# Kernel tuning notes

Hardware: AMD Instinct MI355X
Metric: run time of the kernel (lower is better)

Reference implementation:

```python
import jax, jax.numpy as jnp
import numpy as np

N = 512            # input_size == number of graph nodes (X = I_N)
B = 64             # batch_size
H1, H2, H3 = 128, 64, 32   # hidden3 + 16 must equal 32 + class_nums
OUT = 8            # output_size; OUT*OUT + OUT == 72 (controller out channels)
CLS = 16           # class_nums (one-hot task encoding is 16-dim)


def setup_inputs():
    key = jax.random.key(0)
    ks = jax.random.split(key, 20)

    def u(k, shape, fan_out):
        s = 1.0 / np.sqrt(fan_out)
        return jax.random.uniform(k, shape, jnp.float32, -s, s)

    inp = {
        "adj": jax.random.uniform(ks[0], (B, 2, N, N), jnp.float32),
        "task_id": jax.random.randint(ks[1], (B,), 0, CLS),
    }
    dims = [(N, H1), (H1, H2), (H2, H3), (H3, OUT)]
    i = 2
    for pref in ("p", "n"):
        for l, (fi, fo) in enumerate(dims, 1):
            inp[f"w{l}{pref}"] = u(ks[i], (fi, fo), fo); i += 1
            inp[f"b{l}{pref}"] = u(ks[i], (fo,), fo); i += 1
    # controller: Conv1d(H3+CLS, 72, kernel=1, bias=False) -> stored as [72, H3+CLS]
    inp["wc"] = jax.random.normal(ks[i], (OUT * OUT + OUT, H3 + CLS), jnp.float32) * np.sqrt(2.0 / (OUT * OUT + OUT))
    return inp


def _normalize(adj):
    # D^-1/2 (A + I) D^-1/2, fully vectorized over [B, 2] (original loops in Python)
    a = adj + jnp.eye(adj.shape[-1], dtype=adj.dtype)
    d = a.sum(-1) ** -0.5                       # [B,2,N]
    return d[..., :, None] * a * d[..., None, :]


def _leaky(x):
    return jnp.where(x >= 0, x, 0.2 * x)


def _gcn_branch(feat, ws, bs):
    # feat: [B,N,N] normalized adjacency; X = I_N so first support = W1
    x = jnp.eye(N, dtype=feat.dtype)
    for i, (w, b) in enumerate(zip(ws, bs)):
        x = jnp.matmul(feat, jnp.matmul(x, w)) + b   # [B,N,fo]
        if i < len(ws) - 1:
            x = _leaky(x)
        if i == len(ws) - 2:
            conv3 = x
    return conv3, x                                  # ([B,N,H3], [B,N,OUT])


def _dcl(conv3, task_enc, conv4, wc):
    # conv3: [B,N,H3]; conv4: [B,N,OUT]; task_enc: [B,CLS]
    x_feat = conv3.mean(axis=1)                       # AdaptiveAvgPool1d over nodes -> [B,H3]
    x_cond = jnp.concatenate([x_feat, task_enc], 1)   # [B,H3+CLS]
    params = x_cond @ wc.T                            # [B,72]
    w = params[:, :OUT * OUT].reshape(B, OUT, OUT)    # per-sample dynamic head weights
    b = params[:, OUT * OUT:]                         # [B,OUT]
    # head_inputs = conv4.view(1,-1,N) with groups=B grouped conv1d (kernel 1)
    head = conv4.reshape(B, OUT, N)
    logits = jnp.einsum('boi,bin->bon', w, head) + b[..., None]   # [B,OUT,N]
    return logits.reshape(B, N, OUT)                  # faithful to torch reshape(N_,H_,-1)


def _forward(adj, task_id, w1p, b1p, w2p, b2p, w3p, b3p, w4p, b4p,
             w1n, b1n, w2n, b2n, w3n, b3n, w4n, b4n, wc):
    adj_n = _normalize(adj)
    feat_p, feat_n = adj_n[:, 0], adj_n[:, 1]
    p3, p4 = _gcn_branch(feat_p, [w1p, w2p, w3p, w4p], [b1p, b2p, b3p, b4p])
    n3, n4 = _gcn_branch(feat_n, [w1n, w2n, w3n, w4n], [b1n, b2n, b3n, b4n])
    te = jax.nn.one_hot(task_id, CLS, dtype=adj.dtype)   # encoding_task
    lp = _dcl(p3, te, p4, wc)
    ln = _dcl(n3, te, n4, wc)
    cc = jnp.concatenate([lp, ln], -1).reshape(-1, 2, N, OUT)  # [B,2,N,OUT]
    # F.dropout treated as identity (eval-mode determinism for reference)
    xm = jnp.matmul(cc, jnp.swapaxes(cc, -1, -2))              # [B,2,N,N]
    return jax.nn.log_sigmoid(xm) * -1.0


def reference(adj, task_id, w1p, b1p, w2p, b2p, w3p, b3p, w4p, b4p,
              w1n, b1n, w2n, b2n, w3n, b3n, w4n, b4n, wc):
    return _forward(adj, task_id, w1p, b1p, w2p, b2p, w3p, b3p, w4p, b4p,
                    w1n, b1n, w2n, b2n, w3n, b3n, w4n, b4n, wc)
```

## Files before the change

### kernel.cpp

```cpp
#include <hip/hip_runtime.h>
#include <math.h>

#define NN 512
#define NBC 128

typedef __attribute__((ext_vector_type(8))) __bf16 v8bf;
typedef __attribute__((ext_vector_type(4))) float v4f;

__device__ __forceinline__ void bsplit(float v, unsigned short& h, unsigned short& l) {
    unsigned u  = __builtin_bit_cast(unsigned, v);
    unsigned hb = (u + 0x7fffu + ((u >> 16) & 1u)) & 0xffff0000u;
    float hf    = __builtin_bit_cast(float, hb);
    h = (unsigned short)(hb >> 16);
    float lof   = v - hf;
    unsigned ul = __builtin_bit_cast(unsigned, lof);
    l = (unsigned short)((ul + 0x7fffu + ((ul >> 16) & 1u)) >> 16);
}

__global__ __launch_bounds__(256) void k_rowsum(const float* __restrict__ adj,
                                                float* __restrict__ dinv) {
    int wave = blockIdx.x * 4 + (threadIdx.x >> 6);
    int lane = threadIdx.x & 63;
    const float4* row = (const float4*)(adj + (size_t)wave * NN);
    float4 v0 = row[lane], v1 = row[lane + 64];
    float s = v0.x + v0.y + v0.z + v0.w + v1.x + v1.y + v1.z + v1.w;
    #pragma unroll
    for (int off = 32; off; off >>= 1) s += __shfl_down(s, off, 64);
    if (lane == 0) dinv[wave] = rsqrtf(1.0f + s);
}

__global__ __launch_bounds__(256) void k_convert(const float* __restrict__ adj,
    const float* __restrict__ dinv, unsigned short* __restrict__ anh,
    unsigned short* __restrict__ anl)
{
    unsigned gid = blockIdx.x * 256 + threadIdx.x;
    unsigned e = gid * 4;
    unsigned bc = e >> 18, rem = e & 0x3ffffu;
    unsigned i = rem >> 9, j = rem & 511u;
    float4 a = *(const float4*)(adj + (size_t)e);
    float di = dinv[bc * NN + i];
    const float4 dj = *(const float4*)(dinv + bc * NN + j);
    float v0 = di * dj.x * (a.x + ((j + 0) == i ? 1.f : 0.f));
    float v1 = di * dj.y * (a.y + ((j + 1) == i ? 1.f : 0.f));
    float v2 = di * dj.z * (a.z + ((j + 2) == i ? 1.f : 0.f));
    float v3 = di * dj.w * (a.w + ((j + 3) == i ? 1.f : 0.f));
    ushort4 hh, ll;
    bsplit(v0, hh.x, ll.x); bsplit(v1, hh.y, ll.y);
    bsplit(v2, hh.z, ll.z); bsplit(v3, hh.w, ll.w);
    *(ushort4*)(anh + e) = hh;
    *(ushort4*)(anl + e) = ll;
}

struct WJob  { const float* w; unsigned short* dh; unsigned short* dl; int HI; int HO; int HOP; };
struct WJobs { WJob j[8]; };
__global__ __launch_bounds__(256) void k_wprep(WJobs jobs) {
    WJob jb = jobs.j[blockIdx.y];
    int idx = blockIdx.x * 256 + threadIdx.x;
    if (idx >= jb.HOP * jb.HI) return;
    int h = idx / jb.HI, p = idx % jb.HI;
    float v = (h < jb.HO) ? jb.w[p * jb.HO + h] : 0.f;
    unsigned short hh, ll; bsplit(v, hh, ll);
    jb.dh[idx] = hh; jb.dl[idx] = ll;
}

template<int BN, int OUTW, bool SHAREDZ, bool ACT, bool WBF>
__global__ __launch_bounds__(256, 2) void k_mfma(
    const unsigned short* __restrict__ anh_, const unsigned short* __restrict__ anl_,
    const unsigned short* __restrict__ zh_,  const unsigned short* __restrict__ zl_,
    const float* __restrict__ bp, const float* __restrict__ bn,
    float* __restrict__ xf, unsigned short* __restrict__ xh, unsigned short* __restrict__ xl)
{
    constexpr int C = BN / 16;
    const int bc = blockIdx.y, rb = blockIdx.x;
    const int t = threadIdx.x, w = t >> 6, lane = t & 63;
    const int m0 = lane & 15, quad = lane >> 4;
    const int rowbase = rb * 128 + w * 32;
    const int s = SHAREDZ ? (bc & 1) : bc;
    const unsigned short* pa_h = anh_ + ((size_t)bc * NN + rowbase + m0) * NN + quad * 8;
    const unsigned short* pa_l = anl_ + ((size_t)bc * NN + rowbase + m0) * NN + quad * 8;
    const unsigned short* pz_h = zh_ + ((size_t)s * BN + m0) * NN + quad * 8;
    const unsigned short* pz_l = zl_ + ((size_t)s * BN + m0) * NN + quad * 8;
    v4f acc[2][C];
    #pragma unroll
    for (int r = 0; r < 2; ++r)
        #pragma unroll
        for (int c = 0; c < C; ++c) acc[r][c] = (v4f){0.f, 0.f, 0.f, 0.f};

    for (int kb = 0; kb < 16; ++kb) {
        const int ko = kb * 32;
        v8bf zfh[C], zfl[C];
        #pragma unroll
        for (int c = 0; c < C; ++c) {
            zfh[c] = *(const v8bf*)(pz_h + (size_t)(c * 16) * NN + ko);
            zfl[c] = *(const v8bf*)(pz_l + (size_t)(c * 16) * NN + ko);
        }
        #pragma unroll
        for (int r = 0; r < 2; ++r) {
            v8bf ah = *(const v8bf*)(pa_h + (size_t)(r * 16) * NN + ko);
            v8bf al = *(const v8bf*)(pa_l + (size_t)(r * 16) * NN + ko);
            #pragma unroll
            for (int c = 0; c < C; ++c) {
                acc[r][c] = __builtin_amdgcn_mfma_f32_16x16x32_bf16(ah, zfh[c], acc[r][c], 0, 0, 0);
                acc[r][c] = __builtin_amdgcn_mfma_f32_16x16x32_bf16(ah, zfl[c], acc[r][c], 0, 0, 0);
                acc[r][c] = __builtin_amdgcn_mfma_f32_16x16x32_bf16(al, zfh[c], acc[r][c], 0, 0, 0);
            }
        }
    }
    const float* bias = (bc & 1) ? bn : bp;
    #pragma unroll
    for (int r = 0; r < 2; ++r)
        #pragma unroll
        for (int c = 0; c < C; ++c) {
            int col = c * 16 + m0;
            if (OUTW < BN && col >= OUTW) continue;
            float bv = bias[col];
            #pragma unroll
            for (int reg = 0; reg < 4; ++reg) {
                int row = rowbase + r * 16 + quad * 4 + reg;
                float v = acc[r][c][reg] + bv;
                if (ACT) v = v >= 0.f ? v : 0.2f * v;
                size_t oi = ((size_t)bc * NN + row) * OUTW + col;
                if (xf) xf[oi] = v;
                if (WBF) {
                    unsigned short hh, ll; bsplit(v, hh, ll);
                    xh[oi] = hh; xl[oi] = ll;
                }
            }
        }
}

template<int HI, int HOP>
__global__ __launch_bounds__(256) void k_zgemm(
    const unsigned short* __restrict__ wth, const unsigned short* __restrict__ wtl,
    const unsigned short* __restrict__ xh_, const unsigned short* __restrict__ xl_,
    unsigned short* __restrict__ zh_, unsigned short* __restrict__ zl_)
{
    constexpr int MT = HOP / 16, JW = 4 / MT, NT = 8 / JW;
    const int bc = blockIdx.y, jb = blockIdx.x;
    const int t = threadIdx.x, w = t >> 6, lane = t & 63;
    const int m0 = lane & 15, quad = lane >> 4;
    const int mt = w % MT, jseg = w / MT;
    const int n0 = jb * 128 + jseg * (128 / JW);
    const int s = bc & 1;
    const unsigned short* pw_h = wth + ((size_t)s * HOP + mt * 16 + m0) * HI + quad * 8;
    const unsigned short* pw_l = wtl + ((size_t)s * HOP + mt * 16 + m0) * HI + quad * 8;
    const unsigned short* px_h = xh_ + ((size_t)bc * NN + n0 + m0) * HI + quad * 8;
    const unsigned short* px_l = xl_ + ((size_t)bc * NN + n0 + m0) * HI + quad * 8;
    v4f acc[NT];
    #pragma unroll
    for (int c = 0; c < NT; ++c) acc[c] = (v4f){0.f, 0.f, 0.f, 0.f};
    #pragma unroll
    for (int ks = 0; ks < HI / 32; ++ks) {
        const int ko = ks * 32;
        v8bf awh = *(const v8bf*)(pw_h + ko);
        v8bf awl = *(const v8bf*)(pw_l + ko);
        #pragma unroll
        for (int c = 0; c < NT; ++c) {
            v8bf bxh = *(const v8bf*)(px_h + (size_t)(c * 16) * HI + ko);
            v8bf bxl = *(const v8bf*)(px_l + (size_t)(c * 16) * HI + ko);
            acc[c] = __builtin_amdgcn_mfma_f32_16x16x32_bf16(awh, bxh, acc[c], 0, 0, 0);
            acc[c] = __builtin_amdgcn_mfma_f32_16x16x32_bf16(awh, bxl, acc[c], 0, 0, 0);
            acc[c] = __builtin_amdgcn_mfma_f32_16x16x32_bf16(awl, bxh, acc[c], 0, 0, 0);
        }
    }
    #pragma unroll
    for (int c = 0; c < NT; ++c) {
        int j = n0 + c * 16 + m0;
        #pragma unroll
        for (int reg = 0; reg < 4; ++reg) {
            int h = mt * 16 + quad * 4 + reg;
            unsigned short hh, ll; bsplit(acc[c][reg], hh, ll);
            size_t oi = ((size_t)bc * HOP + h) * NN + j;
            zh_[oi] = hh; zl_[oi] = ll;
        }
    }
}

template<int H, int HP, bool SHARED, bool ACT>
__global__ __launch_bounds__(256) void k_biggemm(
    const float* __restrict__ adj, const float* __restrict__ zcg,
    const float* __restrict__ wp, const float* __restrict__ wn,
    const float* __restrict__ bp, const float* __restrict__ bn,
    const float* __restrict__ dinv, float* __restrict__ xout)
{
    constexpr int CPT = HP / 16;
    constexpr int KT = 64;
    __shared__ float a_s[64 * 68];
    __shared__ float z_s[KT * H];
    const int bc = blockIdx.y;
    const int rt = blockIdx.x;
    const int t  = threadIdx.x;
    const int tx = t & 15, ty = t >> 4;
    const float* A    = adj + (size_t)bc * NN * NN + (size_t)rt * 64 * NN;
    const float* dloc = dinv + bc * NN;
    const float* ZG   = SHARED ? ((bc & 1) ? wn : wp) : (zcg + (size_t)bc * NN * H);
    const float* bias = (bc & 1) ? bn : bp;
    float acc[4][CPT];
    #pragma unroll
    for (int r = 0; r < 4; ++r)
        #pragma unroll
        for (int u = 0; u < CPT; ++u) acc[r][u] = 0.f;
    for (int kb = 0; kb < NN; kb += KT) {
        __syncthreads();
        #pragma unroll
        for (int l = 0; l < 4; ++l) {
            int idx = t + l * 256;
            int r = idx >> 4, q = idx & 15;
            float4 v = *(const float4*)(A + (size_t)r * NN + kb + q * 4);
            *(float4*)(a_s + r * 68 + q * 4) = v;
        }
        constexpr int NZ4 = KT * H / 4;
        for (int idx = t; idx < NZ4; idx += 256) {
            int k = idx / (H / 4), hq = idx % (H / 4);
            float4 v = *(const float4*)(ZG + (size_t)(kb + k) * H + hq * 4);
            if (SHARED) {
                float dk = dloc[kb + k];
                v.x *= dk; v.y *= dk; v.z *= dk; v.w *= dk;
            }
            *(float4*)(z_s + k * H + hq * 4) = v;
        }
        __syncthreads();
        #pragma unroll 8
        for (int k = 0; k < KT; ++k) {
            float ar[4];
            #pragma unroll
            for (int r = 0; r < 4; ++r) ar[r] = a_s[(ty * 4 + r) * 68 + k];
            float zv[CPT];
            #pragma unroll
            for (int u = 0; u < CPT; ++u) {
                int h = tx * CPT + u;
                if (H < HP && h >= H) h = 0;
                zv[u] = z_s[k * H + h];
            }
            #pragma unroll
            for (int r = 0; r < 4; ++r)
                #pragma unroll
                for (int u = 0; u < CPT; ++u)
                    acc[r][u] += ar[r] * zv[u];
        }
    }
    #pragma unroll
    for (int r = 0; r < 4; ++r) {
        int i = rt * 64 + ty * 4 + r;
        float di = dloc[i];
        #pragma unroll
        for (int u = 0; u < CPT; ++u) {
            int h = tx * CPT + u;
            if (H < HP && h >= H) continue;
            float self = SHARED ? di * ZG[(size_t)i * H + h] : ZG[(size_t)i * H + h];
            float v = di * (acc[r][u] + self) + bias[h];
            if (ACT) v = v >= 0.f ? v : 0.2f * v;
            xout[((size_t)bc * NN + i) * H + h] = v;
        }
    }
}
// ... 86 lines not shown
        #pragma unroll
        for (int j = 0; j < 32; ++j) s += wr[j] * xf[j];
        pr[t] = s;
    }
    __syncthreads();
    const float* X4 = x4 + (size_t)bc * 4096;
    float* Lb = L + (size_t)bc * 4096;
    #pragma unroll
    for (int rep = 0; rep < 2; ++rep) {
        int n = rep * 256 + t;
        float hi[8];
        #pragma unroll
        for (int i = 0; i < 8; ++i) hi[i] = X4[i * 512 + n];
        #pragma unroll
        for (int o = 0; o < 8; ++o) {
            float s = pr[64 + o];
            #pragma unroll
            for (int i = 0; i < 8; ++i) s += pr[o * 8 + i] * hi[i];
            Lb[o * 512 + n] = s;
        }
    }
}

#define SCP 520
__global__ __launch_bounds__(256) void k_final(const float* __restrict__ L,
                                               float* __restrict__ out)
{
    __shared__ float scT[8 * SCP];
    const int bcid = blockIdx.y;
    const int b = bcid >> 1, c = bcid & 1;
    const int nt = blockIdx.x, t = threadIdx.x;
    const float* Lp = L + (size_t)(b * 2) * 4096;
    const float* Ln = Lp + 4096;
    for (int rep = 0; rep < 16; ++rep) {
        int e = rep * 256 + t;
        int f = c * 4096 + e;
        int n = f >> 4, k = f & 15;
        float v = (k < 8) ? Lp[n * 8 + k] : Ln[n * 8 + k - 8];
        scT[(e & 7) * SCP + (e >> 3)] = v;
    }
    __syncthreads();
    const int tx = t & 63, ty = t >> 6;
    const int n0 = nt * 32 + ty * 8;
    float cn[8][8];
    #pragma unroll
    for (int o = 0; o < 8; ++o)
        #pragma unroll
        for (int i = 0; i < 8; ++i) cn[i][o] = scT[o * SCP + n0 + i];
    float* ob = out + (size_t)bcid * NN * NN;
    #pragma unroll 2
    for (int mg = 0; mg < 8; ++mg) {
        int m = tx + mg * 64;
        float cm[8];
        #pragma unroll
        for (int o = 0; o < 8; ++o) cm[o] = scT[o * SCP + m];
        #pragma unroll
        for (int i = 0; i < 8; ++i) {
            float s = 0.f;
            #pragma unroll
            for (int o = 0; o < 8; ++o) s += cn[i][o] * cm[o];
            float r = fmaxf(-s, 0.f) + __logf(1.0f + __expf(-fabsf(s)));
            ob[(size_t)(n0 + i) * NN + m] = r;
        }
    }
}

extern "C" void kernel_launch(void* const* d_in, const int* in_sizes, int n_in,
                              void* d_out, int out_size, void* d_ws, size_t ws_size,
                              hipStream_t stream)
{
    const float* adj = (const float*)d_in[0];
    const int*  task = (const int*)d_in[1];
    const float* w1p = (const float*)d_in[2];  const float* b1p = (const float*)d_in[3];
    const float* w2p = (const float*)d_in[4];  const float* b2p = (const float*)d_in[5];
    const float* w3p = (const float*)d_in[6];  const float* b3p = (const float*)d_in[7];
    const float* w4p = (const float*)d_in[8];  const float* b4p = (const float*)d_in[9];
    const float* w1n = (const float*)d_in[10]; const float* b1n = (const float*)d_in[11];
    const float* w2n = (const float*)d_in[12]; const float* b2n = (const float*)d_in[13];
    const float* w3n = (const float*)d_in[14]; const float* b3n = (const float*)d_in[15];
    const float* w4n = (const float*)d_in[16]; const float* b4n = (const float*)d_in[17];
    const float* wc  = (const float*)d_in[18];
    (void)in_sizes; (void)n_in; (void)out_size;

    const size_t NEED = 198004736ull;
    if (ws_size >= NEED) {
        char* base = (char*)d_ws;
        float*          dinv = (float*)(base + 0);
        unsigned short* anh  = (unsigned short*)(base + 262144);
        unsigned short* anl  = (unsigned short*)(base + 67371008);
        unsigned short* zt1h = (unsigned short*)(base + 134479872);
        unsigned short* zt1l = (unsigned short*)(base + 134742016);
        unsigned short* wt2h = (unsigned short*)(base + 135004160);
        unsigned short* wt2l = (unsigned short*)(base + 135036928);
        unsigned short* wt3h = (unsigned short*)(base + 135069696);
        unsigned short* wt3l = (unsigned short*)(base + 135077888);
        unsigned short* wt4h = (unsigned short*)(base + 135086080);
        unsigned short* wt4l = (unsigned short*)(base + 135088128);
        unsigned short* x1h  = (unsigned short*)(base + 135090176);
        unsigned short* x1l  = (unsigned short*)(base + 151867392);
        unsigned short* zt2h = (unsigned short*)(base + 168644608);
        unsigned short* zt2l = (unsigned short*)(base + 177033216);
        float*          x3f  = (float*)(base + 185421824);
        float*          x4f  = (float*)(base + 193810432);
        float*          L    = (float*)(base + 195907584);
        unsigned short* x2h = x1h,  *x2l = x1l;
        unsigned short* x3h = x1h,  *x3l = x1l;
        unsigned short* zt3h = zt2h, *zt3l = zt2l;
        unsigned short* zt4h = zt2h, *zt4l = zt2l;

        k_rowsum<<<dim3(NBC * NN / 4), 256, 0, stream>>>(adj, dinv);
        k_convert<<<dim3(32768), 256, 0, stream>>>(adj, dinv, anh, anl);
        WJobs jobs;
        jobs.j[0] = {w1p, zt1h,          zt1l,          512, 128, 128};
        jobs.j[1] = {w1n, zt1h + 65536,  zt1l + 65536,  512, 128, 128};
        jobs.j[2] = {w2p, wt2h,          wt2l,          128,  64,  64};
        jobs.j[3] = {w2n, wt2h + 8192,   wt2l + 8192,   128,  64,  64};
        jobs.j[4] = {w3p, wt3h,          wt3l,           64,  32,  32};
        jobs.j[5] = {w3n, wt3h + 2048,   wt3l + 2048,    64,  32,  32};
        jobs.j[6] = {w4p, wt4h,          wt4l,           32,   8,  16};
        jobs.j[7] = {w4n, wt4h + 512,    wt4l + 512,     32,   8,  16};
        k_wprep<<<dim3(256, 8), 256, 0, stream>>>(jobs);

        k_mfma<128, 128, true,  true,  true ><<<dim3(4, NBC), 256, 0, stream>>>(
            anh, anl, zt1h, zt1l, b1p, b1n, nullptr, x1h, x1l);
        k_zgemm<128, 64><<<dim3(4, NBC), 256, 0, stream>>>(wt2h, wt2l, x1h, x1l, zt2h, zt2l);
        k_mfma<64, 64, false, true,  true ><<<dim3(4, NBC), 256, 0, stream>>>(
            anh, anl, zt2h, zt2l, b2p, b2n, nullptr, x2h, x2l);
        k_zgemm<64, 32><<<dim3(4, NBC), 256, 0, stream>>>(wt3h, wt3l, x2h, x2l, zt3h, zt3l);
        k_mfma<32, 32, false, true,  true ><<<dim3(4, NBC), 256, 0, stream>>>(
            anh, anl, zt3h, zt3l, b3p, b3n, x3f, x3h, x3l);
        k_zgemm<32, 16><<<dim3(4, NBC), 256, 0, stream>>>(wt4h, wt4l, x3h, x3l, zt4h, zt4l);
        k_mfma<16, 8, false, false, false><<<dim3(4, NBC), 256, 0, stream>>>(
            anh, anl, zt4h, zt4l, b4p, b4n, x4f, nullptr, nullptr);
        k_dcl<<<dim3(NBC), 256, 0, stream>>>(x3f, x4f, wc, task, L);
        k_final<<<dim3(16, NBC), 256, 0, stream>>>(L, (float*)d_out);
    } else {
        float* ws   = (float*)d_ws;
        float* dinv = ws;
        float* XA   = ws + 65536;
        float* X3   = XA + 8388608;
        float* X4   = X3 + 2097152;
        float* L    = X4 + 524288;
        float* ZC   = L  + 524288;
        k_rowsum<<<dim3(NBC * NN / 4), 256, 0, stream>>>(adj, dinv);
        k_biggemm<128,128,true ,true ><<<dim3(8,128), 256, 0, stream>>>(adj, nullptr, w1p, w1n, b1p, b1n, dinv, XA);
        k_smallgemm<128,64><<<dim3(16,128), 256, 0, stream>>>(XA, w2p, w2n, dinv, ZC);
        k_biggemm<64,64,false,true ><<<dim3(8,128), 256, 0, stream>>>(adj, ZC, nullptr, nullptr, b2p, b2n, dinv, XA);
        k_smallgemm<64,32><<<dim3(16,128), 256, 0, stream>>>(XA, w3p, w3n, dinv, ZC);
        k_biggemm<32,32,false,true ><<<dim3(8,128), 256, 0, stream>>>(adj, ZC, nullptr, nullptr, b3p, b3n, dinv, X3);
        k_smallgemm<32,8><<<dim3(16,128), 256, 0, stream>>>(X3, w4p, w4n, dinv, ZC);
        k_biggemm<8,16,false,false><<<dim3(8,128), 256, 0, stream>>>(adj, ZC, nullptr, nullptr, b4p, b4n, dinv, X4);
        k_dcl<<<dim3(128), 256, 0, stream>>>(X3, X4, wc, task, L);
        k_final<<<dim3(16,128), 256, 0, stream>>>(L, (float*)d_out);
    }
}
```

Measured before the change: 567.1 us.

## Stage A and Z tiles through LDS with async global-to-LDS double buffering

The split-bf16 MFMA GEMM now loads adjacency and Z tiles into swizzled shared memory with global_load_lds, double-buffered across K steps, instead of each wave reading fragments straight from global memory. Row tiles shrink from 128 to 64 with a 2D wave split across columns, the grid doubles to 8 row blocks, and launch bounds ask for 3 blocks per CU. The aim is to reuse Z across waves, overlap the next tile's loads with the current MFMAs, and raise occupancy. In exchange it adds a barrier every K step, uses more LDS, and makes the XOR swizzle indexing more complex.

```diff
diff --git a/kernel.cpp b/kernel.cpp
--- a/kernel.cpp
+++ b/kernel.cpp
@@ -15,6 +15,12 @@
     float lof   = v - hf;
     unsigned ul = __builtin_bit_cast(unsigned, lof);
     l = (unsigned short)((ul + 0x7fffu + ((ul >> 16) & 1u)) >> 16);
+}
+
+__device__ __forceinline__ void gl_lds16(const unsigned short* g, unsigned short* l) {
+    __builtin_amdgcn_global_load_lds(
+        (const __attribute__((address_space(1))) void*)g,
+        (__attribute__((address_space(3))) void*)l, 16, 0, 0);
 }
 
 __global__ __launch_bounds__(256) void k_rowsum(const float* __restrict__ adj,
@@ -64,40 +70,93 @@
 }
 
 template<int BN, int OUTW, bool SHAREDZ, bool ACT, bool WBF>
-__global__ __launch_bounds__(256, 2) void k_mfma(
+__global__ __launch_bounds__(256, 3) void k_mfma(
     const unsigned short* __restrict__ anh_, const unsigned short* __restrict__ anl_,
     const unsigned short* __restrict__ zh_,  const unsigned short* __restrict__ zl_,
     const float* __restrict__ bp, const float* __restrict__ bn,
     float* __restrict__ xf, unsigned short* __restrict__ xh, unsigned short* __restrict__ xl)
 {
-    constexpr int C = BN / 16;
+    constexpr int WC    = (BN >= 32) ? 2 : 1;
+    constexpr int WR    = 4 / WC;
+    constexpr int RF    = 64 / (WR * 16);
+    constexpr int C     = (BN / WC) / 16;
+    constexpr int ASH   = 64 * 32;
+    constexpr int ZSH   = BN * 32;
+    constexpr int ZPOS  = BN * 4;
+    constexpr int ZCALL = (ZPOS + 255) / 256;
+    constexpr int BUFS  = 2 * ASH + 2 * ZSH;
+    __shared__ __align__(16) unsigned short smem[2][BUFS];
+
     const int bc = blockIdx.y, rb = blockIdx.x;
     const int t = threadIdx.x, w = t >> 6, lane = t & 63;
     const int m0 = lane & 15, quad = lane >> 4;
-    const int rowbase = rb * 128 + w * 32;
+    const int wr = w / WC, wc = w % WC;
     const int s = SHAREDZ ? (bc & 1) : bc;
-    const unsigned short* pa_h = anh_ + ((size_t)bc * NN + rowbase + m0) * NN + quad * 8;
-    const unsigned short* pa_l = anl_ + ((size_t)bc * NN + rowbase + m0) * NN + quad * 8;
-    const unsigned short* pz_h = zh_ + ((size_t)s * BN + m0) * NN + quad * 8;
-    const unsigned short* pz_l = zl_ + ((size_t)s * BN + m0) * NN + quad * 8;
-    v4f acc[2][C];
-    #pragma unroll
-    for (int r = 0; r < 2; ++r)
+
+    const int arow = t >> 2;
+    const int aslot = (t & 3) ^ ((arow >> 1) & 3);
+    const unsigned short* ga_h = anh_ + ((size_t)bc * NN + (size_t)rb * 64 + arow) * NN + aslot * 8;
+    const unsigned short* ga_l = anl_ + ((size_t)bc * NN + (size_t)rb * 64 + arow) * NN + aslot * 8;
+    const unsigned short* gz_h[ZCALL];
+    const unsigned short* gz_l[ZCALL];
+    #pragma unroll
+    for (int q = 0; q < ZCALL; ++q) {
+        int p = q * 256 + t;
+        if (p >= ZPOS) p = 0;
+        int zr = p >> 2, zs = (p & 3) ^ ((zr >> 1) & 3);
+        gz_h[q] = zh_ + ((size_t)s * BN + zr) * NN + zs * 8;
+        gz_l[q] = zl_ + ((size_t)s * BN + zr) * NN + zs * 8;
+    }
+    const int wbase = w * 512;
+
+    int ra[RF]; int rz[C];
+    #pragma unroll
+    for (int r = 0; r < RF; ++r) {
+        int rho = wr * (RF * 16) + r * 16 + m0;
+        ra[r] = rho * 32 + ((quad ^ ((rho >> 1) & 3)) * 8);
+    }
+    #pragma unroll
+    for (int c = 0; c < C; ++c) {
+        int n = wc * (BN / WC) + c * 16 + m0;
+        rz[c] = 2 * ASH + n * 32 + ((quad ^ ((n >> 1) & 3)) * 8);
+    }
+
+    v4f acc[RF][C];
+    #pragma unroll
+    for (int r = 0; r < RF; ++r)
         #pragma unroll
         for (int c = 0; c < C; ++c) acc[r][c] = (v4f){0.f, 0.f, 0.f, 0.f};
 
+    auto STAGE = [&](int b, int kb) {
+        const int ko = kb * 32;
+        unsigned short* base = smem[b];
+        gl_lds16(ga_h + ko, base + wbase);
+        gl_lds16(ga_l + ko, base + ASH + wbase);
+        #pragma unroll
+        for (int q = 0; q < ZCALL; ++q) {
+            if (q * 256 + w * 64 < ZPOS) {
+                gl_lds16(gz_h[q] + ko, base + 2 * ASH + q * 2048 + wbase);
+                gl_lds16(gz_l[q] + ko, base + 2 * ASH + ZSH + q * 2048 + wbase);
+            }
+        }
+    };
+
+    STAGE(0, 0);
+    int buf = 0;
     for (int kb = 0; kb < 16; ++kb) {
-        const int ko = kb * 32;
+        __syncthreads();
+        if (kb < 15) STAGE(buf ^ 1, kb + 1);
+        const unsigned short* bs = smem[buf];
         v8bf zfh[C], zfl[C];
         #pragma unroll
         for (int c = 0; c < C; ++c) {
-            zfh[c] = *(const v8bf*)(pz_h + (size_t)(c * 16) * NN + ko);
-            zfl[c] = *(const v8bf*)(pz_l + (size_t)(c * 16) * NN + ko);
-        }
-        #pragma unroll
-        for (int r = 0; r < 2; ++r) {
-            v8bf ah = *(const v8bf*)(pa_h + (size_t)(r * 16) * NN + ko);
-            v8bf al = *(const v8bf*)(pa_l + (size_t)(r * 16) * NN + ko);
+            zfh[c] = *(const v8bf*)(bs + rz[c]);
+            zfl[c] = *(const v8bf*)(bs + rz[c] + ZSH);
+        }
+        #pragma unroll
+        for (int r = 0; r < RF; ++r) {
+            v8bf ah = *(const v8bf*)(bs + ra[r]);
+            v8bf al = *(const v8bf*)(bs + ra[r] + ASH);
             #pragma unroll
             for (int c = 0; c < C; ++c) {
                 acc[r][c] = __builtin_amdgcn_mfma_f32_16x16x32_bf16(ah, zfh[c], acc[r][c], 0, 0, 0);
@@ -105,18 +164,20 @@
                 acc[r][c] = __builtin_amdgcn_mfma_f32_16x16x32_bf16(al, zfh[c], acc[r][c], 0, 0, 0);
             }
         }
-    }
+        buf ^= 1;
+    }
+
     const float* bias = (bc & 1) ? bn : bp;
     #pragma unroll
-    for (int r = 0; r < 2; ++r)
+    for (int r = 0; r < RF; ++r)
         #pragma unroll
         for (int c = 0; c < C; ++c) {
-            int col = c * 16 + m0;
+            int col = wc * (BN / WC) + c * 16 + m0;
             if (OUTW < BN && col >= OUTW) continue;
             float bv = bias[col];
             #pragma unroll
             for (int reg = 0; reg < 4; ++reg) {
-                int row = rowbase + r * 16 + quad * 4 + reg;
+                int row = rb * 64 + wr * (RF * 16) + r * 16 + quad * 4 + reg;
                 float v = acc[r][c][reg] + bv;
                 if (ACT) v = v >= 0.f ? v : 0.2f * v;
                 size_t oi = ((size_t)bc * NN + row) * OUTW + col;
@@ -462,16 +523,16 @@
         jobs.j[7] = {w4n, wt4h + 512,    wt4l + 512,     32,   8,  16};
         k_wprep<<<dim3(256, 8), 256, 0, stream>>>(jobs);
 
-        k_mfma<128, 128, true,  true,  true ><<<dim3(4, NBC), 256, 0, stream>>>(
+        k_mfma<128, 128, true,  true,  true ><<<dim3(8, NBC), 256, 0, stream>>>(
             anh, anl, zt1h, zt1l, b1p, b1n, nullptr, x1h, x1l);
         k_zgemm<128, 64><<<dim3(4, NBC), 256, 0, stream>>>(wt2h, wt2l, x1h, x1l, zt2h, zt2l);
-        k_mfma<64, 64, false, true,  true ><<<dim3(4, NBC), 256, 0, stream>>>(
+        k_mfma<64, 64, false, true,  true ><<<dim3(8, NBC), 256, 0, stream>>>(
             anh, anl, zt2h, zt2l, b2p, b2n, nullptr, x2h, x2l);
         k_zgemm<64, 32><<<dim3(4, NBC), 256, 0, stream>>>(wt3h, wt3l, x2h, x2l, zt3h, zt3l);
-        k_mfma<32, 32, false, true,  true ><<<dim3(4, NBC), 256, 0, stream>>>(
+        k_mfma<32, 32, false, true,  true ><<<dim3(8, NBC), 256, 0, stream>>>(
             anh, anl, zt3h, zt3l, b3p, b3n, x3f, x3h, x3l);
         k_zgemm<32, 16><<<dim3(4, NBC), 256, 0, stream>>>(wt4h, wt4l, x3h, x3l, zt4h, zt4l);
-        k_mfma<16, 8, false, false, false><<<dim3(4, NBC), 256, 0, stream>>>(
+        k_mfma<16, 8, false, false, false><<<dim3(8, NBC), 256, 0, stream>>>(
             anh, anl, zt4h, zt4l, b4p, b4n, x4f, nullptr, nullptr);
         k_dcl<<<dim3(NBC), 256, 0, stream>>>(x3f, x4f, wc, task, L);
         k_final<<<dim3(16, NBC), 256, 0, stream>>>(L, (float*)d_out);
```

Result: faster. 534.3 us (-5.8%).

## Store bf16 operands in MFMA fragment-major layout and retile GEMM blocks

Applied to the files above, without the earlier changes.

Normalized adjacency, weights, and intermediate activations are written in a fragment-tiled layout (16x32 tiles stored contiguously, in the per-lane order the MFMA wants). Each lane's 16-byte load then becomes fully contiguous across the wave instead of striding across rows. The adjacency GEMM kernels also switch to 64-row blocks with a 2D wave split over rows and columns, twice as many blocks, and per-variant occupancy bounds. The intent is better coalescing and more parallelism, at the cost of more complex index math and scattered 2-byte stores in the epilogues.

```diff
diff --git a/kernel.cpp b/kernel.cpp
--- a/kernel.cpp
+++ b/kernel.cpp
@@ -17,6 +17,11 @@
     l = (unsigned short)((ul + 0x7fffu + ((ul >> 16) & 1u)) >> 16);
 }
 
+__device__ __forceinline__ size_t fragaddr(int n, int k, int kext) {
+    return ((size_t)(n >> 4) * (kext >> 5) + (k >> 5)) * 512
+         + (size_t)(((n & 15) + 16 * ((k >> 3) & 3)) * 8 + (k & 7));
+}
+
 __global__ __launch_bounds__(256) void k_rowsum(const float* __restrict__ adj,
                                                 float* __restrict__ dinv) {
     int wave = blockIdx.x * 4 + (threadIdx.x >> 6);
@@ -33,22 +38,36 @@
     const float* __restrict__ dinv, unsigned short* __restrict__ anh,
     unsigned short* __restrict__ anl)
 {
-    unsigned gid = blockIdx.x * 256 + threadIdx.x;
-    unsigned e = gid * 4;
-    unsigned bc = e >> 18, rem = e & 0x3ffffu;
-    unsigned i = rem >> 9, j = rem & 511u;
-    float4 a = *(const float4*)(adj + (size_t)e);
-    float di = dinv[bc * NN + i];
-    const float4 dj = *(const float4*)(dinv + bc * NN + j);
-    float v0 = di * dj.x * (a.x + ((j + 0) == i ? 1.f : 0.f));
-    float v1 = di * dj.y * (a.y + ((j + 1) == i ? 1.f : 0.f));
-    float v2 = di * dj.z * (a.z + ((j + 2) == i ? 1.f : 0.f));
-    float v3 = di * dj.w * (a.w + ((j + 3) == i ? 1.f : 0.f));
-    ushort4 hh, ll;
-    bsplit(v0, hh.x, ll.x); bsplit(v1, hh.y, ll.y);
-    bsplit(v2, hh.z, ll.z); bsplit(v3, hh.w, ll.w);
-    *(ushort4*)(anh + e) = hh;
-    *(ushort4*)(anl + e) = ll;
+    const int row4 = blockIdx.x;
+    const int bc = row4 >> 7;
+    const int wv = threadIdx.x >> 6, lane = threadIdx.x & 63;
+    const int i = (row4 & 127) * 4 + wv;
+    const int it = i >> 4;
+    const int j0 = lane * 8;
+    const float* arow = adj + ((size_t)bc * NN + i) * NN + j0;
+    float4 a0 = *(const float4*)(arow);
+    float4 a1 = *(const float4*)(arow + 4);
+    const float di = dinv[bc * NN + i];
+    const float4 d0 = *(const float4*)(dinv + bc * NN + j0);
+    const float4 d1 = *(const float4*)(dinv + bc * NN + j0 + 4);
+    float av[8] = { a0.x, a0.y, a0.z, a0.w, a1.x, a1.y, a1.z, a1.w };
+    float dj[8] = { d0.x, d0.y, d0.z, d0.w, d1.x, d1.y, d1.z, d1.w };
+    unsigned pw[4], qw[4];
+    #pragma unroll
+    for (int q = 0; q < 4; ++q) {
+        unsigned short h0, l0, h1, l1;
+        float u0 = di * dj[2*q]     * (av[2*q]     + ((j0 + 2*q)     == i ? 1.f : 0.f));
+        float u1 = di * dj[2*q + 1] * (av[2*q + 1] + ((j0 + 2*q + 1) == i ? 1.f : 0.f));
+        bsplit(u0, h0, l0); bsplit(u1, h1, l1);
+        pw[q] = (unsigned)h0 | ((unsigned)h1 << 16);
+        qw[q] = (unsigned)l0 | ((unsigned)l1 << 16);
+    }
+    size_t oa = (((size_t)(bc * 32 + it)) * 16 + (j0 >> 5)) * 512
+              + (size_t)(((i & 15) + 16 * ((j0 >> 3) & 3)) * 8);
+    uint4 ph; ph.x = pw[0]; ph.y = pw[1]; ph.z = pw[2]; ph.w = pw[3];
+    uint4 pl; pl.x = qw[0]; pl.y = qw[1]; pl.z = qw[2]; pl.w = qw[3];
+    *(uint4*)(anh + oa) = ph;
+    *(uint4*)(anl + oa) = pl;
 }
 
 struct WJob  { const float* w; unsigned short* dh; unsigned short* dl; int HI; int HO; int HOP; };
@@ -60,70 +79,93 @@
     int h = idx / jb.HI, p = idx % jb.HI;
     float v = (h < jb.HO) ? jb.w[p * jb.HO + h] : 0.f;
     unsigned short hh, ll; bsplit(v, hh, ll);
-    jb.dh[idx] = hh; jb.dl[idx] = ll;
-}
-
-template<int BN, int OUTW, bool SHAREDZ, bool ACT, bool WBF>
-__global__ __launch_bounds__(256, 2) void k_mfma(
+    size_t oa = fragaddr(h, p, jb.HI);
+    jb.dh[oa] = hh; jb.dl[oa] = ll;
+}
+
+template<int BN, int OUTW, bool SHAREDZ, bool ACT, bool WBF, int MINW>
+__global__ __launch_bounds__(256, MINW) void k_mfma(
     const unsigned short* __restrict__ anh_, const unsigned short* __restrict__ anl_,
     const unsigned short* __restrict__ zh_,  const unsigned short* __restrict__ zl_,
     const float* __restrict__ bp, const float* __restrict__ bn,
     float* __restrict__ xf, unsigned short* __restrict__ xh, unsigned short* __restrict__ xl)
 {
-    constexpr int C = BN / 16;
+    constexpr int WC = (BN >= 32) ? 2 : 1;
+    constexpr int WR = 4 / WC;
+    constexpr int RF = 64 / (WR * 16);
+    constexpr int C  = (BN / WC) / 16;
     const int bc = blockIdx.y, rb = blockIdx.x;
     const int t = threadIdx.x, w = t >> 6, lane = t & 63;
     const int m0 = lane & 15, quad = lane >> 4;
-    const int rowbase = rb * 128 + w * 32;
+    const int wr = w / WC, wc = w % WC;
     const int s = SHAREDZ ? (bc & 1) : bc;
-    const unsigned short* pa_h = anh_ + ((size_t)bc * NN + rowbase + m0) * NN + quad * 8;
-    const unsigned short* pa_l = anl_ + ((size_t)bc * NN + rowbase + m0) * NN + quad * 8;
-    const unsigned short* pz_h = zh_ + ((size_t)s * BN + m0) * NN + quad * 8;
-    const unsigned short* pz_l = zl_ + ((size_t)s * BN + m0) * NN + quad * 8;
-    v4f acc[2][C];
-    #pragma unroll
-    for (int r = 0; r < 2; ++r)
+
+    const unsigned short* pah[RF]; const unsigned short* pal[RF];
+    #pragma unroll
+    for (int r = 0; r < RF; ++r) {
+        int it = rb * 4 + wr * RF + r;
+        size_t b0 = ((size_t)(bc * 32 + it)) * 8192 + (size_t)(lane * 8);
+        pah[r] = anh_ + b0; pal[r] = anl_ + b0;
+    }
+    const unsigned short* pzh[C]; const unsigned short* pzl[C];
+    #pragma unroll
+    for (int c = 0; c < C; ++c) {
+        int nt = (wc * (BN / WC)) / 16 + c;
+        size_t b0 = ((size_t)(s * (BN / 16) + nt)) * 8192 + (size_t)(lane * 8);
+        pzh[c] = zh_ + b0; pzl[c] = zl_ + b0;
+    }
+
+    v4f acc[RF][C];
+    #pragma unroll
+    for (int r = 0; r < RF; ++r)
         #pragma unroll
         for (int c = 0; c < C; ++c) acc[r][c] = (v4f){0.f, 0.f, 0.f, 0.f};
 
+    #pragma unroll 2
     for (int kb = 0; kb < 16; ++kb) {
-        const int ko = kb * 32;
+        const int ko = kb * 512;
         v8bf zfh[C], zfl[C];
         #pragma unroll
         for (int c = 0; c < C; ++c) {
-            zfh[c] = *(const v8bf*)(pz_h + (size_t)(c * 16) * NN + ko);
-            zfl[c] = *(const v8bf*)(pz_l + (size_t)(c * 16) * NN + ko);
-        }
-        #pragma unroll
-        for (int r = 0; r < 2; ++r) {
-            v8bf ah = *(const v8bf*)(pa_h + (size_t)(r * 16) * NN + ko);
-            v8bf al = *(const v8bf*)(pa_l + (size_t)(r * 16) * NN + ko);
+            zfh[c] = *(const v8bf*)(pzh[c] + ko);
+            zfl[c] = *(const v8bf*)(pzl[c] + ko);
+        }
+        v8bf ahh[RF], all_[RF];
+        #pragma unroll
+        for (int r = 0; r < RF; ++r) {
+            ahh[r]  = *(const v8bf*)(pah[r] + ko);
+            all_[r] = *(const v8bf*)(pal[r] + ko);
+        }
+        #pragma unroll
+        for (int r = 0; r < RF; ++r) {
             #pragma unroll
             for (int c = 0; c < C; ++c) {
-                acc[r][c] = __builtin_amdgcn_mfma_f32_16x16x32_bf16(ah, zfh[c], acc[r][c], 0, 0, 0);
-                acc[r][c] = __builtin_amdgcn_mfma_f32_16x16x32_bf16(ah, zfl[c], acc[r][c], 0, 0, 0);
-                acc[r][c] = __builtin_amdgcn_mfma_f32_16x16x32_bf16(al, zfh[c], acc[r][c], 0, 0, 0);
+                acc[r][c] = __builtin_amdgcn_mfma_f32_16x16x32_bf16(ahh[r],  zfh[c], acc[r][c], 0, 0, 0);
+                acc[r][c] = __builtin_amdgcn_mfma_f32_16x16x32_bf16(ahh[r],  zfl[c], acc[r][c], 0, 0, 0);
+                acc[r][c] = __builtin_amdgcn_mfma_f32_16x16x32_bf16(all_[r], zfh[c], acc[r][c], 0, 0, 0);
             }
         }
     }
+
     const float* bias = (bc & 1) ? bn : bp;
     #pragma unroll
-    for (int r = 0; r < 2; ++r)
+    for (int r = 0; r < RF; ++r)
         #pragma unroll
         for (int c = 0; c < C; ++c) {
-            int col = c * 16 + m0;
+            int col = wc * (BN / WC) + c * 16 + m0;
             if (OUTW < BN && col >= OUTW) continue;
             float bv = bias[col];
             #pragma unroll
             for (int reg = 0; reg < 4; ++reg) {
-                int row = rowbase + r * 16 + quad * 4 + reg;
+                int row = rb * 64 + wr * (RF * 16) + r * 16 + quad * 4 + reg;
                 float v = acc[r][c][reg] + bv;
                 if (ACT) v = v >= 0.f ? v : 0.2f * v;
-                size_t oi = ((size_t)bc * NN + row) * OUTW + col;
-                if (xf) xf[oi] = v;
+                if (xf) xf[((size_t)bc * NN + row) * OUTW + col] = v;
                 if (WBF) {
                     unsigned short hh, ll; bsplit(v, hh, ll);
-                    xh[oi] = hh; xl[oi] = ll;
+                    size_t fo = (((size_t)(bc * 32) + (row >> 4)) * (OUTW / 32) + (col >> 5)) * 512
+                              + (size_t)(((row & 15) + 16 * ((col >> 3) & 3)) * 8 + (col & 7));
+                    xh[fo] = hh; xl[fo] = ll;
                 }
             }
         }
@@ -142,22 +184,27 @@
     const int mt = w % MT, jseg = w / MT;
     const int n0 = jb * 128 + jseg * (128 / JW);
     const int s = bc & 1;
-    const unsigned short* pw_h = wth + ((size_t)s * HOP + mt * 16 + m0) * HI + quad * 8;
-    const unsigned short* pw_l = wtl + ((size_t)s * HOP + mt * 16 + m0) * HI + quad * 8;
-    const unsigned short* px_h = xh_ + ((size_t)bc * NN + n0 + m0) * HI + quad * 8;
-    const unsigned short* px_l = xl_ + ((size_t)bc * NN + n0 + m0) * HI + quad * 8;
+    size_t wb = ((size_t)(s * MT + mt)) * (size_t)((HI / 32) * 512) + (size_t)(lane * 8);
+    const unsigned short* pw_h = wth + wb;
+    const unsigned short* pw_l = wtl + wb;
+    const unsigned short* pxh[NT]; const unsigned short* pxl[NT];
+    #pragma unroll
+    for (int c = 0; c < NT; ++c) {
+        size_t xb = ((size_t)(bc * 32 + (n0 >> 4) + c)) * (size_t)((HI / 32) * 512) + (size_t)(lane * 8);
+        pxh[c] = xh_ + xb; pxl[c] = xl_ + xb;
+    }
     v4f acc[NT];
     #pragma unroll
     for (int c = 0; c < NT; ++c) acc[c] = (v4f){0.f, 0.f, 0.f, 0.f};
     #pragma unroll
     for (int ks = 0; ks < HI / 32; ++ks) {
-        const int ko = ks * 32;
+        const int ko = ks * 512;
         v8bf awh = *(const v8bf*)(pw_h + ko);
         v8bf awl = *(const v8bf*)(pw_l + ko);
         #pragma unroll
         for (int c = 0; c < NT; ++c) {
-            v8bf bxh = *(const v8bf*)(px_h + (size_t)(c * 16) * HI + ko);
-            v8bf bxl = *(const v8bf*)(px_l + (size_t)(c * 16) * HI + ko);
+            v8bf bxh = *(const v8bf*)(pxh[c] + ko);
+            v8bf bxl = *(const v8bf*)(pxl[c] + ko);
             acc[c] = __builtin_amdgcn_mfma_f32_16x16x32_bf16(awh, bxh, acc[c], 0, 0, 0);
             acc[c] = __builtin_amdgcn_mfma_f32_16x16x32_bf16(awh, bxl, acc[c], 0, 0, 0);
             acc[c] = __builtin_amdgcn_mfma_f32_16x16x32_bf16(awl, bxh, acc[c], 0, 0, 0);
@@ -166,11 +213,13 @@
     #pragma unroll
     for (int c = 0; c < NT; ++c) {
         int j = n0 + c * 16 + m0;
+        int jt = j >> 5, jg = (j >> 3) & 3, je = j & 7;
         #pragma unroll
         for (int reg = 0; reg < 4; ++reg) {
             int h = mt * 16 + quad * 4 + reg;
             unsigned short hh, ll; bsplit(acc[c][reg], hh, ll);
-            size_t oi = ((size_t)bc * HOP + h) * NN + j;
+            size_t oi = (((size_t)(bc * MT + mt)) * 16 + jt) * 512
+                      + (size_t)(((h & 15) + 16 * jg) * 8 + je);
             zh_[oi] = hh; zl_[oi] = ll;
         }
     }
@@ -450,7 +499,7 @@
         unsigned short* zt4h = zt2h, *zt4l = zt2l;
 
         k_rowsum<<<dim3(NBC * NN / 4), 256, 0, stream>>>(adj, dinv);
-        k_convert<<<dim3(32768), 256, 0, stream>>>(adj, dinv, anh, anl);
+        k_convert<<<dim3(16384), 256, 0, stream>>>(adj, dinv, anh, anl);
         WJobs jobs;
         jobs.j[0] = {w1p, zt1h,          zt1l,          512, 128, 128};
         jobs.j[1] = {w1n, zt1h + 65536,  zt1l + 65536,  512, 128, 128};
@@ -462,16 +511,16 @@
         jobs.j[7] = {w4n, wt4h + 512,    wt4l + 512,     32,   8,  16};
         k_wprep<<<dim3(256, 8), 256, 0, stream>>>(jobs);
 
-        k_mfma<128, 128, true,  true,  true ><<<dim3(4, NBC), 256, 0, stream>>>(
+        k_mfma<128, 128, true,  true,  true,  3><<<dim3(8, NBC), 256, 0, stream>>>(
             anh, anl, zt1h, zt1l, b1p, b1n, nullptr, x1h, x1l);
         k_zgemm<128, 64><<<dim3(4, NBC), 256, 0, stream>>>(wt2h, wt2l, x1h, x1l, zt2h, zt2l);
-        k_mfma<64, 64, false, true,  true ><<<dim3(4, NBC), 256, 0, stream>>>(
+        k_mfma<64, 64, false, true,  true,  4><<<dim3(8, NBC), 256, 0, stream>>>(
             anh, anl, zt2h, zt2l, b2p, b2n, nullptr, x2h, x2l);
         k_zgemm<64, 32><<<dim3(4, NBC), 256, 0, stream>>>(wt3h, wt3l, x2h, x2l, zt3h, zt3l);
-        k_mfma<32, 32, false, true,  true ><<<dim3(4, NBC), 256, 0, stream>>>(
+        k_mfma<32, 32, false, true,  true,  4><<<dim3(8, NBC), 256, 0, stream>>>(
             anh, anl, zt3h, zt3l, b3p, b3n, x3f, x3h, x3l);
         k_zgemm<32, 16><<<dim3(4, NBC), 256, 0, stream>>>(wt4h, wt4l, x3h, x3l, zt4h, zt4l);
-        k_mfma<16, 8, false, false, false><<<dim3(4, NBC), 256, 0, stream>>>(
+        k_mfma<16, 8, false, false, false, 4><<<dim3(8, NBC), 256, 0, stream>>>(
             anh, anl, zt4h, zt4l, b4p, b4n, x4f, nullptr, nullptr);
         k_dcl<<<dim3(NBC), 256, 0, stream>>>(x3f, x4f, wc, task, L);
         k_final<<<dim3(16, NBC), 256, 0, stream>>>(L, (float*)d_out);
```

Result: no change. 561.5 us (-1.0%).

## Fuse adjacency normalization into MFMA GEMMs with LDS double-buffered tiles

Applied to the files above, without the earlier changes.

Removes the separate pass that wrote normalized adjacency as bf16 hi/lo planes. Each GEMM now reads the fp32 adjacency directly, applies the D^-1/2 scaling and the self-loop, splits to hi/lo bf16 on the fly, and stages the tiles in shared memory. The A and Z tiles are double-buffered in LDS with register prefetch, and the block tiling and occupancy hints change per layer. The aim is to avoid writing and re-reading 128 MB of bf16 planes. In exchange the 128 MB of fp32 adjacency is read and converted four times, once per layer.

```diff
diff --git a/kernel.cpp b/kernel.cpp
--- a/kernel.cpp
+++ b/kernel.cpp
@@ -27,28 +27,6 @@
     #pragma unroll
     for (int off = 32; off; off >>= 1) s += __shfl_down(s, off, 64);
     if (lane == 0) dinv[wave] = rsqrtf(1.0f + s);
-}
-
-__global__ __launch_bounds__(256) void k_convert(const float* __restrict__ adj,
-    const float* __restrict__ dinv, unsigned short* __restrict__ anh,
-    unsigned short* __restrict__ anl)
-{
-    unsigned gid = blockIdx.x * 256 + threadIdx.x;
-    unsigned e = gid * 4;
-    unsigned bc = e >> 18, rem = e & 0x3ffffu;
-    unsigned i = rem >> 9, j = rem & 511u;
-    float4 a = *(const float4*)(adj + (size_t)e);
-    float di = dinv[bc * NN + i];
-    const float4 dj = *(const float4*)(dinv + bc * NN + j);
-    float v0 = di * dj.x * (a.x + ((j + 0) == i ? 1.f : 0.f));
-    float v1 = di * dj.y * (a.y + ((j + 1) == i ? 1.f : 0.f));
-    float v2 = di * dj.z * (a.z + ((j + 2) == i ? 1.f : 0.f));
-    float v3 = di * dj.w * (a.w + ((j + 3) == i ? 1.f : 0.f));
-    ushort4 hh, ll;
-    bsplit(v0, hh.x, ll.x); bsplit(v1, hh.y, ll.y);
-    bsplit(v2, hh.z, ll.z); bsplit(v3, hh.w, ll.w);
-    *(ushort4*)(anh + e) = hh;
-    *(ushort4*)(anl + e) = ll;
 }
 
 struct WJob  { const float* w; unsigned short* dh; unsigned short* dl; int HI; int HO; int HOP; };
@@ -63,41 +41,129 @@
     jb.dh[idx] = hh; jb.dl[idx] = ll;
 }
 
-template<int BN, int OUTW, bool SHAREDZ, bool ACT, bool WBF>
-__global__ __launch_bounds__(256, 2) void k_mfma(
-    const unsigned short* __restrict__ anh_, const unsigned short* __restrict__ anl_,
+template<int BN, int OUTW, bool SHAREDZ, bool ACT, bool WBF, int MINW>
+__global__ __launch_bounds__(256, MINW) void k_mfma(
+    const float* __restrict__ adj, const float* __restrict__ dinv,
     const unsigned short* __restrict__ zh_,  const unsigned short* __restrict__ zl_,
     const float* __restrict__ bp, const float* __restrict__ bn,
     float* __restrict__ xf, unsigned short* __restrict__ xh, unsigned short* __restrict__ xl)
 {
-    constexpr int C = BN / 16;
+    constexpr int WC  = (BN >= 32) ? 2 : 1;
+    constexpr int WR  = 4 / WC;
+    constexpr int RF  = 64 / (WR * 16);
+    constexpr int C   = (BN / WC) / 16;
+    constexpr int AS  = 40;
+    constexpr int APL = 64 * AS;
+    constexpr int ABUF = 2 * APL;
+    constexpr int ZPL = BN * AS;
+    constexpr int ZBUF = 2 * ZPL;
+    constexpr int ZCH = (BN == 128) ? 2 : 1;
+    constexpr int ZTHREADS = (BN >= 64) ? 256 : BN * 4;
+    __shared__ __align__(16) unsigned short sm[2 * ABUF + 2 * ZBUF];
+    __shared__ float dls[512];
+
     const int bc = blockIdx.y, rb = blockIdx.x;
     const int t = threadIdx.x, w = t >> 6, lane = t & 63;
     const int m0 = lane & 15, quad = lane >> 4;
-    const int rowbase = rb * 128 + w * 32;
+    const int wr = w / WC, wcc = w % WC;
     const int s = SHAREDZ ? (bc & 1) : bc;
-    const unsigned short* pa_h = anh_ + ((size_t)bc * NN + rowbase + m0) * NN + quad * 8;
-    const unsigned short* pa_l = anl_ + ((size_t)bc * NN + rowbase + m0) * NN + quad * 8;
-    const unsigned short* pz_h = zh_ + ((size_t)s * BN + m0) * NN + quad * 8;
-    const unsigned short* pz_l = zl_ + ((size_t)s * BN + m0) * NN + quad * 8;
-    v4f acc[2][C];
-    #pragma unroll
-    for (int r = 0; r < 2; ++r)
+
+    const int arow = t >> 2, c8 = t & 3;
+    const int gcol0 = c8 * 8;
+    const int growi = rb * 64 + arow;
+    const float* gA = adj + ((size_t)bc * NN + growi) * NN + gcol0;
+    const float di = dinv[bc * NN + growi];
+    const bool zact = (ZTHREADS == 256) || (t < ZTHREADS);
+
+    float4 aR[3][2];
+    uint4  zRh[2][ZCH], zRl[2][ZCH];
+
+    auto LOADA = [&](int kb, int slot) {
+        aR[slot][0] = *(const float4*)(gA + (size_t)kb * 32);
+        aR[slot][1] = *(const float4*)(gA + (size_t)kb * 32 + 4);
+    };
+    auto LOADZ = [&](int kb, int slot) {
+        if (zact) {
+            #pragma unroll
+            for (int q = 0; q < ZCH; ++q) {
+                int ci = (ZCH == 2) ? (t * 2 + q) : t;
+                int zn = ci >> 2, zk = (ci & 3) * 8;
+                size_t go = ((size_t)s * BN + zn) * NN + (size_t)kb * 32 + zk;
+                zRh[slot][q] = *(const uint4*)(zh_ + go);
+                zRl[slot][q] = *(const uint4*)(zl_ + go);
+            }
+        }
+    };
+    auto WRITEA = [&](int kb, int buf) {
+        const int slot = kb % 3;
+        const float4 d0 = *(const float4*)(&dls[kb * 32 + gcol0]);
+        const float4 d1 = *(const float4*)(&dls[kb * 32 + gcol0 + 4]);
+        float av[8] = { aR[slot][0].x, aR[slot][0].y, aR[slot][0].z, aR[slot][0].w,
+                        aR[slot][1].x, aR[slot][1].y, aR[slot][1].z, aR[slot][1].w };
+        float dj[8] = { d0.x, d0.y, d0.z, d0.w, d1.x, d1.y, d1.z, d1.w };
+        unsigned pw[4], qw[4];
+        const int jb0 = kb * 32 + gcol0;
+        #pragma unroll
+        for (int q = 0; q < 4; ++q) {
+            unsigned short h0, l0, h1, l1;
+            float u0 = di * dj[2*q]     * (av[2*q]     + ((jb0 + 2*q)     == growi ? 1.f : 0.f));
+            float u1 = di * dj[2*q + 1] * (av[2*q + 1] + ((jb0 + 2*q + 1) == growi ? 1.f : 0.f));
+            bsplit(u0, h0, l0); bsplit(u1, h1, l1);
+            pw[q] = (unsigned)h0 | ((unsigned)h1 << 16);
+            qw[q] = (unsigned)l0 | ((unsigned)l1 << 16);
+        }
+        uint4 ph; ph.x = pw[0]; ph.y = pw[1]; ph.z = pw[2]; ph.w = pw[3];
+        uint4 pl; pl.x = qw[0]; pl.y = qw[1]; pl.z = qw[2]; pl.w = qw[3];
+        *(uint4*)(&sm[buf * ABUF + arow * AS + gcol0])       = ph;
+        *(uint4*)(&sm[buf * ABUF + APL + arow * AS + gcol0]) = pl;
+    };
+    auto WRITEZ = [&](int slot, int buf) {
+        if (zact) {
+            #pragma unroll
+            for (int q = 0; q < ZCH; ++q) {
+                int ci = (ZCH == 2) ? (t * 2 + q) : t;
+                int zn = ci >> 2, zk = (ci & 3) * 8;
+                *(uint4*)(&sm[2 * ABUF + buf * ZBUF + zn * AS + zk])       = zRh[slot][q];
+                *(uint4*)(&sm[2 * ABUF + buf * ZBUF + ZPL + zn * AS + zk]) = zRl[slot][q];
+            }
+        }
+    };
+
+    v4f acc[RF][C];
+    #pragma unroll
+    for (int r = 0; r < RF; ++r)
         #pragma unroll
         for (int c = 0; c < C; ++c) acc[r][c] = (v4f){0.f, 0.f, 0.f, 0.f};
 
+    if (t < 128) *(float4*)(&dls[t * 4]) = *(const float4*)(dinv + bc * NN + t * 4);
+    LOADA(0, 0); LOADA(1, 1); LOADA(2, 2);
+    LOADZ(0, 0); LOADZ(1, 1);
+    __syncthreads();
+    WRITEA(0, 0); WRITEZ(0, 0);
+    asm volatile("" ::: "memory");
+    __builtin_amdgcn_s_barrier();
+    asm volatile("" ::: "memory");
+
+    #pragma unroll
     for (int kb = 0; kb < 16; ++kb) {
-        const int ko = kb * 32;
+        const int cur = kb & 1;
+        if (kb + 3 < 16) LOADA(kb + 3, (kb + 3) % 3);
+        if (kb + 2 < 16) LOADZ(kb + 2, cur);
+
+        const unsigned short* ab = sm + (size_t)(cur * ABUF);
+        const unsigned short* zb = sm + (size_t)(2 * ABUF + cur * ZBUF);
         v8bf zfh[C], zfl[C];
         #pragma unroll
         for (int c = 0; c < C; ++c) {
-            zfh[c] = *(const v8bf*)(pz_h + (size_t)(c * 16) * NN + ko);
-            zfl[c] = *(const v8bf*)(pz_l + (size_t)(c * 16) * NN + ko);
-        }
-        #pragma unroll
-        for (int r = 0; r < 2; ++r) {
-            v8bf ah = *(const v8bf*)(pa_h + (size_t)(r * 16) * NN + ko);
-            v8bf al = *(const v8bf*)(pa_l + (size_t)(r * 16) * NN + ko);
+            int n = wcc * (BN / WC) + c * 16 + m0;
+            zfh[c] = *(const v8bf*)(zb + n * AS + quad * 8);
+            zfl[c] = *(const v8bf*)(zb + ZPL + n * AS + quad * 8);
+        }
+        #pragma unroll
+        for (int r = 0; r < RF; ++r) {
+            int rho = wr * (RF * 16) + r * 16 + m0;
+            v8bf ah = *(const v8bf*)(ab + rho * AS + quad * 8);
+            v8bf al = *(const v8bf*)(ab + APL + rho * AS + quad * 8);
             #pragma unroll
             for (int c = 0; c < C; ++c) {
                 acc[r][c] = __builtin_amdgcn_mfma_f32_16x16x32_bf16(ah, zfh[c], acc[r][c], 0, 0, 0);
@@ -105,18 +171,26 @@
                 acc[r][c] = __builtin_amdgcn_mfma_f32_16x16x32_bf16(al, zfh[c], acc[r][c], 0, 0, 0);
             }
         }
-    }
+        if (kb + 1 < 16) {
+            WRITEA(kb + 1, cur ^ 1);
+            WRITEZ(cur ^ 1, cur ^ 1);
+            asm volatile("" ::: "memory");
+            __builtin_amdgcn_s_barrier();
+            asm volatile("" ::: "memory");
+        }
+    }
+
     const float* bias = (bc & 1) ? bn : bp;
     #pragma unroll
-    for (int r = 0; r < 2; ++r)
+    for (int r = 0; r < RF; ++r)
         #pragma unroll
         for (int c = 0; c < C; ++c) {
-            int col = c * 16 + m0;
+            int col = wcc * (BN / WC) + c * 16 + m0;
             if (OUTW < BN && col >= OUTW) continue;
             float bv = bias[col];
             #pragma unroll
             for (int reg = 0; reg < 4; ++reg) {
-                int row = rowbase + r * 16 + quad * 4 + reg;
+                int row = rb * 64 + wr * (RF * 16) + r * 16 + quad * 4 + reg;
                 float v = acc[r][c][reg] + bv;
                 if (ACT) v = v >= 0.f ? v : 0.2f * v;
                 size_t oi = ((size_t)bc * NN + row) * OUTW + col;
@@ -423,34 +497,31 @@
     const float* wc  = (const float*)d_in[18];
     (void)in_sizes; (void)n_in; (void)out_size;
 
-    const size_t NEED = 198004736ull;
+    const size_t NEED = 63787008ull;
     if (ws_size >= NEED) {
         char* base = (char*)d_ws;
         float*          dinv = (float*)(base + 0);
-        unsigned short* anh  = (unsigned short*)(base + 262144);
-        unsigned short* anl  = (unsigned short*)(base + 67371008);
-        unsigned short* zt1h = (unsigned short*)(base + 134479872);
-        unsigned short* zt1l = (unsigned short*)(base + 134742016);
-        unsigned short* wt2h = (unsigned short*)(base + 135004160);
-        unsigned short* wt2l = (unsigned short*)(base + 135036928);
-        unsigned short* wt3h = (unsigned short*)(base + 135069696);
-        unsigned short* wt3l = (unsigned short*)(base + 135077888);
-        unsigned short* wt4h = (unsigned short*)(base + 135086080);
-        unsigned short* wt4l = (unsigned short*)(base + 135088128);
-        unsigned short* x1h  = (unsigned short*)(base + 135090176);
-        unsigned short* x1l  = (unsigned short*)(base + 151867392);
-        unsigned short* zt2h = (unsigned short*)(base + 168644608);
-        unsigned short* zt2l = (unsigned short*)(base + 177033216);
-        float*          x3f  = (float*)(base + 185421824);
-        float*          x4f  = (float*)(base + 193810432);
-        float*          L    = (float*)(base + 195907584);
+        unsigned short* zt1h = (unsigned short*)(base + 262144);
+        unsigned short* zt1l = (unsigned short*)(base + 524288);
+        unsigned short* wt2h = (unsigned short*)(base + 786432);
+        unsigned short* wt2l = (unsigned short*)(base + 819200);
+        unsigned short* wt3h = (unsigned short*)(base + 851968);
+        unsigned short* wt3l = (unsigned short*)(base + 860160);
+        unsigned short* wt4h = (unsigned short*)(base + 868352);
+        unsigned short* wt4l = (unsigned short*)(base + 870400);
+        unsigned short* x1h  = (unsigned short*)(base + 872448);
+        unsigned short* x1l  = (unsigned short*)(base + 17649664);
+        unsigned short* zt2h = (unsigned short*)(base + 34426880);
+        unsigned short* zt2l = (unsigned short*)(base + 42815488);
+        float*          x3f  = (float*)(base + 51204096);
+        float*          x4f  = (float*)(base + 59592704);
+        float*          L    = (float*)(base + 61689856);
         unsigned short* x2h = x1h,  *x2l = x1l;
         unsigned short* x3h = x1h,  *x3l = x1l;
         unsigned short* zt3h = zt2h, *zt3l = zt2l;
         unsigned short* zt4h = zt2h, *zt4l = zt2l;
 
         k_rowsum<<<dim3(NBC * NN / 4), 256, 0, stream>>>(adj, dinv);
-        k_convert<<<dim3(32768), 256, 0, stream>>>(adj, dinv, anh, anl);
         WJobs jobs;
         jobs.j[0] = {w1p, zt1h,          zt1l,          512, 128, 128};
         jobs.j[1] = {w1n, zt1h + 65536,  zt1l + 65536,  512, 128, 128};
@@ -462,17 +533,17 @@
         jobs.j[7] = {w4n, wt4h + 512,    wt4l + 512,     32,   8,  16};
         k_wprep<<<dim3(256, 8), 256, 0, stream>>>(jobs);
 
-        k_mfma<128, 128, true,  true,  true ><<<dim3(4, NBC), 256, 0, stream>>>(
-            anh, anl, zt1h, zt1l, b1p, b1n, nullptr, x1h, x1l);
+        k_mfma<128, 128, true,  true,  true,  2><<<dim3(8, NBC), 256, 0, stream>>>(
+            adj, dinv, zt1h, zt1l, b1p, b1n, nullptr, x1h, x1l);
         k_zgemm<128, 64><<<dim3(4, NBC), 256, 0, stream>>>(wt2h, wt2l, x1h, x1l, zt2h, zt2l);
-        k_mfma<64, 64, false, true,  true ><<<dim3(4, NBC), 256, 0, stream>>>(
-            anh, anl, zt2h, zt2l, b2p, b2n, nullptr, x2h, x2l);
+        k_mfma<64, 64, false, true,  true,  3><<<dim3(8, NBC), 256, 0, stream>>>(
+            adj, dinv, zt2h, zt2l, b2p, b2n, nullptr, x2h, x2l);
         k_zgemm<64, 32><<<dim3(4, NBC), 256, 0, stream>>>(wt3h, wt3l, x2h, x2l, zt3h, zt3l);
-        k_mfma<32, 32, false, true,  true ><<<dim3(4, NBC), 256, 0, stream>>>(
-            anh, anl, zt3h, zt3l, b3p, b3n, x3f, x3h, x3l);
+        k_mfma<32, 32, false, true,  true,  4><<<dim3(8, NBC), 256, 0, stream>>>(
+            adj, dinv, zt3h, zt3l, b3p, b3n, x3f, x3h, x3l);
         k_zgemm<32, 16><<<dim3(4, NBC), 256, 0, stream>>>(wt4h, wt4l, x3h, x3l, zt4h, zt4l);
-        k_mfma<16, 8, false, false, false><<<dim3(4, NBC), 256, 0, stream>>>(
-            anh, anl, zt4h, zt4l, b4p, b4n, x4f, nullptr, nullptr);
+        k_mfma<16, 8, false, false, false, 4><<<dim3(8, NBC), 256, 0, stream>>>(
+            adj, dinv, zt4h, zt4l, b4p, b4n, x4f, nullptr, nullptr);
         k_dcl<<<dim3(NBC), 256, 0, stream>>>(x3f, x4f, wc, task, L);
         k_final<<<dim3(16, NBC), 256, 0, stream>>>(L, (float*)d_out);
     } else {
```

Result: no change. 559.9 us (-1.3%).
